# Kernel optimization log

Measured on AMD Instinct MI355X. Metric: run time of the kernel, lower is better.

Reference implementation:

```python
import jax, jax.numpy as jnp
import numpy as np

N = 8192
IN_C = 128
OUT_C = 64
ALPHA = 0.5  # LeakyReLU negative slope
NEG_INF = -9e15


def _xavier(key, shape, gain=1.414):
    fan_in, fan_out = shape[0], shape[-1]
    bound = gain * np.sqrt(6.0 / (fan_in + fan_out))
    return jax.random.uniform(key, shape, jnp.float32, -bound, bound)


def setup_inputs() -> dict:
    key = jax.random.key(0)
    k1, k2, k3, k4 = jax.random.split(key, 4)
    h = jax.random.normal(k1, (N, IN_C), jnp.float32)
    adj = jax.random.randint(k2, (N, N), 0, 2, jnp.int32)
    W = _xavier(k3, (IN_C, OUT_C))
    a = _xavier(k4, (2 * OUT_C, 1))
    return {"h": h, "adj": adj, "W": W, "a": a}


def reference(h, adj, W, a):
    # Wh: [N, out]
    Wh = h @ W
    a1 = a[:OUT_C, 0]   # [out]
    a2 = a[OUT_C:, 0]   # [out]
    # additive attention score e[i, j] = leakyrelu((Wh a1)_i + (Wh a2)_j)
    e = jax.nn.leaky_relu(
        (Wh @ a1)[:, None] + (Wh @ a2)[None, :], negative_slope=ALPHA
    )  # [N, N]
    scores = jnp.where(adj > 0, e, NEG_INF)
    attention = jax.nn.softmax(scores, axis=1)  # masked row softmax
    h_prime = attention @ Wh                    # [N, out]
    return jax.nn.leaky_relu(h_prime, negative_slope=ALPHA)  # concat=True path
```

## Files before the change

kernel.cpp:

```cpp
#include <hip/hip_runtime.h>
#include <hip/hip_bf16.h>

#define NN 8192
#define INC 128
#define OUTC 64

typedef __attribute__((ext_vector_type(8))) short bf16x8;
typedef __attribute__((ext_vector_type(4))) float f32x4;
typedef __attribute__((ext_vector_type(4))) int i32x4;

static __device__ __forceinline__ unsigned short f2bf(float x) {
    unsigned int u = __builtin_bit_cast(unsigned int, x);
    u += 0x7fffu + ((u >> 16) & 1u);
    return (unsigned short)(u >> 16);
}

__global__ __launch_bounds__(256) void ka_pack(const int* __restrict__ adj,
                                               unsigned long long* __restrict__ msk)
{
    const int lane = threadIdx.x & 63;
    const int wid  = (blockIdx.x * 256 + threadIdx.x) >> 6;
    const int l16  = lane & 15;
    const int g16  = lane >> 4;
#pragma unroll 4
    for (int i = 0; i < 32; ++i) {
        const size_t base = ((size_t)wid * 32 + i) * 256;
        i32x4 v = *(const i32x4*)(adj + base + 4 * lane);
        unsigned int nib = (v[0] > 0 ? 1u : 0u) | (v[1] > 0 ? 2u : 0u)
                         | (v[2] > 0 ? 4u : 0u) | (v[3] > 0 ? 8u : 0u);
        unsigned long long m = (unsigned long long)nib << (4 * l16);
        m |= __shfl_xor(m, 1, 64);
        m |= __shfl_xor(m, 2, 64);
        m |= __shfl_xor(m, 4, 64);
        m |= __shfl_xor(m, 8, 64);
        if (l16 == 0) msk[base / 64 + g16] = m;
    }
}

__global__ __launch_bounds__(512) void k1_wh(const float* __restrict__ h,
                                             const float* __restrict__ W,
                                             const float* __restrict__ a,
                                             unsigned short* __restrict__ whF,
                                             float* __restrict__ f,
                                             float* __restrict__ g)
{
    const int wave = threadIdx.x >> 6;
    const int ch   = threadIdx.x & 63;
    const int seg  = blockIdx.x;
    const int row  = seg * 8 + wave;
    const f32x4* h4 = (const f32x4*)(h + (size_t)row * INC);
    float acc = 0.f;
#pragma unroll 8
    for (int k4 = 0; k4 < INC / 4; ++k4) {
        f32x4 hv = h4[k4];
        acc += hv[0] * W[(k4 * 4 + 0) * OUTC + ch];
        acc += hv[1] * W[(k4 * 4 + 1) * OUTC + ch];
        acc += hv[2] * W[(k4 * 4 + 2) * OUTC + ch];
        acc += hv[3] * W[(k4 * 4 + 3) * OUTC + ch];
    }
    __shared__ unsigned short tr[64][8];
    tr[ch][wave] = f2bf(acc);

    float v1 = acc * a[ch];
    float v2 = acc * a[64 + ch];
#pragma unroll
    for (int m = 1; m < 64; m <<= 1) {
        v1 += __shfl_xor(v1, m, 64);
        v2 += __shfl_xor(v2, m, 64);
    }
    if (ch == 0) { f[row] = v1; g[row] = v2; }
    __syncthreads();
    if (threadIdx.x < 64) {
        bf16x8 frag = *(const bf16x8*)&tr[threadIdx.x][0];
        *(bf16x8*)(whF + ((size_t)seg * 64 + threadIdx.x) * 8) = frag;
    }
}

__global__ __launch_bounds__(256) void k2_gmax(const float* __restrict__ g,
                                               float* __restrict__ gmax)
{
    __shared__ float red[256];
    float m = -1e30f;
    for (int i = threadIdx.x; i < NN; i += 256) m = fmaxf(m, g[i]);
    red[threadIdx.x] = m;
    __syncthreads();
    for (int s = 128; s > 0; s >>= 1) {
        if ((int)threadIdx.x < s) red[threadIdx.x] = fmaxf(red[threadIdx.x], red[threadIdx.x + s]);
        __syncthreads();
    }
    if (threadIdx.x == 0) *gmax = red[0];
}

__global__ __launch_bounds__(256) void k3_attn(const unsigned int* __restrict__ msk,
                                               const unsigned short* __restrict__ whF,
                                               const float* __restrict__ f,
                                               const float* __restrict__ g,
                                               const float* __restrict__ gmaxp,
                                               float* __restrict__ accP,
                                               float* __restrict__ lP,
                                               int colsPerChunk)
{
    const int lane = threadIdx.x & 63;
    const int wave = threadIdx.x >> 6;
    const int lr16 = lane & 15;
    const int kg   = lane >> 4;
    const int rowBase = blockIdx.x * 64 + wave * 16;
    const int r = rowBase + lr16;
    const int chunk = blockIdx.y;
    const int jStart = chunk * colsPerChunk;

    const float L2E = 1.4426950408889634f;
    const float fr = f[r];
    const float gmax = *gmaxp;
    float mm = fr + gmax;
    mm = fmaxf(mm, 0.5f * mm);
    const float mL  = mm * L2E;
    const float frE = fr * L2E - mL;
    const float hm  = -0.5f * mL;

    f32x4 acc0 = {0.f, 0.f, 0.f, 0.f};
    f32x4 acc1 = {0.f, 0.f, 0.f, 0.f};
    f32x4 acc2 = {0.f, 0.f, 0.f, 0.f};
    f32x4 acc3 = {0.f, 0.f, 0.f, 0.f};
    f32x4 accl = {0.f, 0.f, 0.f, 0.f};
    bf16x8 ones;
#pragma unroll
    for (int t = 0; t < 8; ++t) ones[t] = (short)0x3F80;

    const unsigned int* mrow = msk + (size_t)r * (NN / 32);

#pragma unroll 2
    for (int j0 = jStart; j0 < jStart + colsPerChunk; j0 += 32) {
        const int jl = j0 + kg * 8;
        unsigned int mw = mrow[j0 >> 5];
        unsigned int myb = (mw >> (kg * 8)) & 0xffu;
        f32x4 g0  = *(const f32x4*)(g + jl);
        f32x4 g1  = *(const f32x4*)(g + jl + 4);
        const size_t segB = (size_t)((j0 >> 3) + kg) * 64;
        bf16x8 b0 = *(const bf16x8*)(whF + (segB +  0 + lr16) * 8);
        bf16x8 b1 = *(const bf16x8*)(whF + (segB + 16 + lr16) * 8);
        bf16x8 b2 = *(const bf16x8*)(whF + (segB + 32 + lr16) * 8);
        bf16x8 b3 = *(const bf16x8*)(whF + (segB + 48 + lr16) * 8);

        bf16x8 af;
#pragma unroll
        for (int t = 0; t < 8; ++t) {
            float gj = (t < 4) ? g0[t] : g1[t - 4];
            float se = __builtin_fmaf(gj, L2E, frE);
            float u  = __builtin_fmaf(0.5f, se, hm);
            float w  = __builtin_amdgcn_exp2f(fmaxf(se, u));
            w = (myb & (1u << t)) ? w : 0.f;
            af[t] = (short)f2bf(w);
        }
        acc0 = __builtin_amdgcn_mfma_f32_16x16x32_bf16(af, b0, acc0, 0, 0, 0);
        acc1 = __builtin_amdgcn_mfma_f32_16x16x32_bf16(af, b1, acc1, 0, 0, 0);
        acc2 = __builtin_amdgcn_mfma_f32_16x16x32_bf16(af, b2, acc2, 0, 0, 0);
        acc3 = __builtin_amdgcn_mfma_f32_16x16x32_bf16(af, b3, acc3, 0, 0, 0);
        accl = __builtin_amdgcn_mfma_f32_16x16x32_bf16(af, ones, accl, 0, 0, 0);
    }

    if (lr16 == 0) {
#pragma unroll
        for (int q = 0; q < 4; ++q)
            lP[(size_t)chunk * NN + rowBase + kg * 4 + q] = accl[q];
    }

    float* ap = accP + (size_t)chunk * NN * OUTC;
#pragma unroll
    for (int q = 0; q < 4; ++q) {
        const int rm = rowBase + kg * 4 + q;
        ap[(size_t)rm * OUTC +  0 + lr16] = acc0[q];
        ap[(size_t)rm * OUTC + 16 + lr16] = acc1[q];
        ap[(size_t)rm * OUTC + 32 + lr16] = acc2[q];
        ap[(size_t)rm * OUTC + 48 + lr16] = acc3[q];
    }
}

__global__ __launch_bounds__(256) void k4_final(const float* __restrict__ accP,
                                                const float* __restrict__ lP,
                                                float* __restrict__ out, int js)
{
    const int gid = blockIdx.x * 256 + threadIdx.x;
    const int row = gid >> 6;
    const int ch  = gid & 63;
    float av = 0.f, lv = 0.f;
    for (int c = 0; c < js; ++c) {
        av += accP[((size_t)c * NN + row) * OUTC + ch];
        lv += lP[(size_t)c * NN + row];
    }
    if (lv == 0.f) lv = 1.f;
    const float hv = av / lv;
    out[(size_t)row * OUTC + ch] = fmaxf(hv, 0.5f * hv);
}

extern "C" void kernel_launch(void* const* d_in, const int* in_sizes, int n_in,
                              void* d_out, int out_size, void* d_ws, size_t ws_size,
                              hipStream_t stream)
{
    const float* h   = (const float*)d_in[0];
    const int*   adj = (const int*)d_in[1];
    const float* W   = (const float*)d_in[2];
    const float* a   = (const float*)d_in[3];
    float* out = (float*)d_out;

    char* ws = (char*)d_ws;
    unsigned short* whF = (unsigned short*)ws;
    size_t off = (size_t)OUTC * NN * sizeof(unsigned short);
    float* f = (float*)(ws + off); off += (size_t)NN * 4;
    float* g = (float*)(ws + off); off += (size_t)NN * 4;
    float* gmax = (float*)(ws + off); off += 256;
    unsigned long long* msk = (unsigned long long*)(ws + off);
    off += (size_t)NN * NN / 8;

    const size_t perChunk = (size_t)NN * OUTC * 4 + (size_t)NN * 4;
    int js = 16;
    while (js > 1 && off + (size_t)js * perChunk > ws_size) js >>= 1;
    float* accP = (float*)(ws + off); off += (size_t)js * NN * OUTC * 4;
    float* lP   = (float*)(ws + off);

    ka_pack<<<dim3(2048), 256, 0, stream>>>(adj, msk);
    k1_wh<<<dim3(NN / 8), 512, 0, stream>>>(h, W, a, whF, f, g);
    k2_gmax<<<1, 256, 0, stream>>>(g, gmax);
    const int colsPerChunk = NN / js;
    k3_attn<<<dim3(NN / 64, js), 256, 0, stream>>>((const unsigned int*)msk, whF,
                                                   f, g, gmax, accP, lP, colsPerChunk);
    k4_final<<<dim3(NN * OUTC / 256), 256, 0, stream>>>(accP, lP, out, js);
}
```

Measured before the change: 441.5 us.

## Stage Wh tiles through double-buffered LDS in attention kernel with register prefetch

The attention kernel now loads each 64-column slice of the bf16 Wh matrix cooperatively into shared memory, double-buffered, so the four waves of a block share one copy instead of each fetching it from global memory. The next slice's Wh, mask words and g values are prefetched into registers while the current slice's MFMAs run. Chunk count is fixed at 16 with 512 columns per chunk, and the launch bound adds a minimum of 4 blocks. The cost is two barriers per slice plus the LDS traffic, and the fixed split drops the fallback that sized chunks to the workspace.

```diff
diff --git a/kernel.cpp b/kernel.cpp
--- a/kernel.cpp
+++ b/kernel.cpp
@@ -91,23 +91,25 @@
     if (threadIdx.x == 0) *gmax = red[0];
 }
 
-__global__ __launch_bounds__(256) void k3_attn(const unsigned int* __restrict__ msk,
-                                               const unsigned short* __restrict__ whF,
-                                               const float* __restrict__ f,
-                                               const float* __restrict__ g,
-                                               const float* __restrict__ gmaxp,
-                                               float* __restrict__ accP,
-                                               float* __restrict__ lP,
-                                               int colsPerChunk)
-{
-    const int lane = threadIdx.x & 63;
-    const int wave = threadIdx.x >> 6;
+__global__ __launch_bounds__(256, 4) void k3_attn(const unsigned int* __restrict__ msk,
+                                                  const unsigned short* __restrict__ whF,
+                                                  const float* __restrict__ f,
+                                                  const float* __restrict__ g,
+                                                  const float* __restrict__ gmaxp,
+                                                  float* __restrict__ accP,
+                                                  float* __restrict__ lP)
+{
+    const int tid  = threadIdx.x;
+    const int lane = tid & 63;
+    const int wave = tid >> 6;
     const int lr16 = lane & 15;
     const int kg   = lane >> 4;
     const int rowBase = blockIdx.x * 64 + wave * 16;
     const int r = rowBase + lr16;
     const int chunk = blockIdx.y;
-    const int jStart = chunk * colsPerChunk;
+    const int jStart = chunk * 512;
+
+    __shared__ __align__(16) unsigned short lds[2][4096];
 
     const float L2E = 1.4426950408889634f;
     const float fr = f[r];
@@ -129,34 +131,81 @@
 
     const unsigned int* mrow = msk + (size_t)r * (NN / 32);
 
+    {
+        const unsigned short* gs = whF + (size_t)(jStart >> 3) * 512;
+        bf16x8 s0 = *(const bf16x8*)(gs + tid * 8);
+        bf16x8 s1 = *(const bf16x8*)(gs + (tid + 256) * 8);
+        *(bf16x8*)&lds[0][tid * 8] = s0;
+        *(bf16x8*)&lds[0][(tid + 256) * 8] = s1;
+    }
+    uint2 mqC = *(const uint2*)(mrow + (jStart >> 5));
+    f32x4 gC[4];
+    gC[0] = *(const f32x4*)(g + jStart + kg * 8);
+    gC[1] = *(const f32x4*)(g + jStart + kg * 8 + 4);
+    gC[2] = *(const f32x4*)(g + jStart + 32 + kg * 8);
+    gC[3] = *(const f32x4*)(g + jStart + 32 + kg * 8 + 4);
+    __syncthreads();
+
 #pragma unroll 2
-    for (int j0 = jStart; j0 < jStart + colsPerChunk; j0 += 32) {
-        const int jl = j0 + kg * 8;
-        unsigned int mw = mrow[j0 >> 5];
-        unsigned int myb = (mw >> (kg * 8)) & 0xffu;
-        f32x4 g0  = *(const f32x4*)(g + jl);
-        f32x4 g1  = *(const f32x4*)(g + jl + 4);
-        const size_t segB = (size_t)((j0 >> 3) + kg) * 64;
-        bf16x8 b0 = *(const bf16x8*)(whF + (segB +  0 + lr16) * 8);
-        bf16x8 b1 = *(const bf16x8*)(whF + (segB + 16 + lr16) * 8);
-        bf16x8 b2 = *(const bf16x8*)(whF + (segB + 32 + lr16) * 8);
-        bf16x8 b3 = *(const bf16x8*)(whF + (segB + 48 + lr16) * 8);
-
-        bf16x8 af;
-#pragma unroll
-        for (int t = 0; t < 8; ++t) {
-            float gj = (t < 4) ? g0[t] : g1[t - 4];
-            float se = __builtin_fmaf(gj, L2E, frE);
-            float u  = __builtin_fmaf(0.5f, se, hm);
-            float w  = __builtin_amdgcn_exp2f(fmaxf(se, u));
-            w = (myb & (1u << t)) ? w : 0.f;
-            af[t] = (short)f2bf(w);
-        }
-        acc0 = __builtin_amdgcn_mfma_f32_16x16x32_bf16(af, b0, acc0, 0, 0, 0);
-        acc1 = __builtin_amdgcn_mfma_f32_16x16x32_bf16(af, b1, acc1, 0, 0, 0);
-        acc2 = __builtin_amdgcn_mfma_f32_16x16x32_bf16(af, b2, acc2, 0, 0, 0);
-        acc3 = __builtin_amdgcn_mfma_f32_16x16x32_bf16(af, b3, acc3, 0, 0, 0);
-        accl = __builtin_amdgcn_mfma_f32_16x16x32_bf16(af, ones, accl, 0, 0, 0);
+    for (int sub = 0; sub < 8; ++sub) {
+        const int cur = sub & 1;
+        const int j0 = jStart + sub * 64;
+
+        bf16x8 n0, n1;
+        uint2 mqN;
+        f32x4 gN[4];
+        if (sub < 7) {
+            const unsigned short* gs = whF + (size_t)((j0 + 64) >> 3) * 512;
+            n0 = *(const bf16x8*)(gs + tid * 8);
+            n1 = *(const bf16x8*)(gs + (tid + 256) * 8);
+            mqN = *(const uint2*)(mrow + ((j0 + 64) >> 5));
+            gN[0] = *(const f32x4*)(g + j0 + 64 + kg * 8);
+            gN[1] = *(const f32x4*)(g + j0 + 64 + kg * 8 + 4);
+            gN[2] = *(const f32x4*)(g + j0 + 96 + kg * 8);
+            gN[3] = *(const f32x4*)(g + j0 + 96 + kg * 8 + 4);
+        }
+
+#pragma unroll
+        for (int s2 = 0; s2 < 2; ++s2) {
+            const unsigned int mwv = s2 ? mqC.y : mqC.x;
+            const unsigned int myb = (mwv >> (kg * 8)) & 0xffu;
+            const f32x4 G0 = gC[s2 * 2 + 0];
+            const f32x4 G1 = gC[s2 * 2 + 1];
+
+            const int slb = (s2 * 4 + kg) * 64;
+            bf16x8 b0 = *(const bf16x8*)&lds[cur][(slb +  0 + lr16) * 8];
+            bf16x8 b1 = *(const bf16x8*)&lds[cur][(slb + 16 + lr16) * 8];
+            bf16x8 b2 = *(const bf16x8*)&lds[cur][(slb + 32 + lr16) * 8];
+            bf16x8 b3 = *(const bf16x8*)&lds[cur][(slb + 48 + lr16) * 8];
+
+            bf16x8 af;
+#pragma unroll
+            for (int t = 0; t < 8; ++t) {
+                float gj = (t < 4) ? G0[t] : G1[t - 4];
+                float se = __builtin_fmaf(gj, L2E, frE);
+                float u  = __builtin_fmaf(0.5f, se, hm);
+                float w  = __builtin_amdgcn_exp2f(fmaxf(se, u));
+                w = (myb & (1u << t)) ? w : 0.f;
+                af[t] = (short)f2bf(w);
+            }
+            acc0 = __builtin_amdgcn_mfma_f32_16x16x32_bf16(af, b0, acc0, 0, 0, 0);
+            acc1 = __builtin_amdgcn_mfma_f32_16x16x32_bf16(af, b1, acc1, 0, 0, 0);
+            acc2 = __builtin_amdgcn_mfma_f32_16x16x32_bf16(af, b2, acc2, 0, 0, 0);
+            acc3 = __builtin_amdgcn_mfma_f32_16x16x32_bf16(af, b3, acc3, 0, 0, 0);
+            accl = __builtin_amdgcn_mfma_f32_16x16x32_bf16(af, ones, accl, 0, 0, 0);
+        }
+
+        __syncthreads();
+        if (sub < 7) {
+            *(bf16x8*)&lds[1 - cur][tid * 8] = n0;
+            *(bf16x8*)&lds[1 - cur][(tid + 256) * 8] = n1;
+        }
+        __syncthreads();
+
+        if (sub < 7) {
+            mqC = mqN;
+            gC[0] = gN[0]; gC[1] = gN[1]; gC[2] = gN[2]; gC[3] = gN[3];
+        }
     }
 
     if (lr16 == 0) {
@@ -212,17 +261,14 @@
     unsigned long long* msk = (unsigned long long*)(ws + off);
     off += (size_t)NN * NN / 8;
 
-    const size_t perChunk = (size_t)NN * OUTC * 4 + (size_t)NN * 4;
-    int js = 16;
-    while (js > 1 && off + (size_t)js * perChunk > ws_size) js >>= 1;
+    const int js = 16;
     float* accP = (float*)(ws + off); off += (size_t)js * NN * OUTC * 4;
     float* lP   = (float*)(ws + off);
 
     ka_pack<<<dim3(2048), 256, 0, stream>>>(adj, msk);
     k1_wh<<<dim3(NN / 8), 512, 0, stream>>>(h, W, a, whF, f, g);
     k2_gmax<<<1, 256, 0, stream>>>(g, gmax);
-    const int colsPerChunk = NN / js;
     k3_attn<<<dim3(NN / 64, js), 256, 0, stream>>>((const unsigned int*)msk, whF,
-                                                   f, g, gmax, accP, lP, colsPerChunk);
+                                                   f, g, gmax, accP, lP);
     k4_final<<<dim3(NN * OUTC / 256), 256, 0, stream>>>(accP, lP, out, js);
 }
```

Result: faster. 430.0 us (-2.6%).
